# Kernel tuning notes

Hardware: AMD Instinct MI355X
Metric: run time of the kernel (lower is better)

## Reference

```python
import jax, jax.numpy as jnp
import numpy as np
from jax import lax

# Model hyperparameters (from module source: D_state=2, Expand=1; mamba-ssm defaults)
B_, C_, H_, W_ = 16, 128, 96, 96
D_MODEL = C_
D_INNER = 1 * D_MODEL          # expand = 1
D_STATE = 2
DT_RANK = (D_MODEL + 15) // 16  # ceil(d_model/16) = 8
D_CONV = 4
OUT_C = 128
LN_EPS = 1e-5


def setup_inputs() -> dict:
    key = jax.random.key(0)
    ks = jax.random.split(key, 10)
    s = 0.02
    x = jax.random.normal(ks[0], (B_, C_, H_, W_), dtype=jnp.float32)
    in_proj_w = jax.random.normal(ks[1], (2 * D_INNER, D_MODEL), dtype=jnp.float32) * s
    conv_w = jax.random.normal(ks[2], (D_INNER, 1, D_CONV), dtype=jnp.float32) * s
    conv_b = jnp.zeros((D_INNER,), dtype=jnp.float32)
    x_proj_w = jax.random.normal(ks[3], (DT_RANK + 2 * D_STATE, D_INNER), dtype=jnp.float32) * s
    dt_proj_w = jax.random.normal(ks[4], (D_INNER, DT_RANK), dtype=jnp.float32) * s
    # softplus^{-1}(0.01) so initial dt ~ 0.01 (standard mamba init)
    dt_proj_b = jnp.full((D_INNER,), float(np.log(np.expm1(0.01))), dtype=jnp.float32)
    A_log = jnp.log(jnp.broadcast_to(jnp.arange(1, D_STATE + 1, dtype=jnp.float32), (D_INNER, D_STATE)))
    D_param = jnp.ones((D_INNER,), dtype=jnp.float32)
    out_proj_w = jax.random.normal(ks[5], (OUT_C, D_INNER), dtype=jnp.float32) * s
    ln_gamma = jnp.ones((OUT_C,), dtype=jnp.float32)
    ln_beta = jnp.zeros((OUT_C,), dtype=jnp.float32)
    return {
        "x": x, "in_proj_w": in_proj_w, "conv_w": conv_w, "conv_b": conv_b,
        "x_proj_w": x_proj_w, "dt_proj_w": dt_proj_w, "dt_proj_b": dt_proj_b,
        "A_log": A_log, "D_param": D_param, "out_proj_w": out_proj_w,
        "ln_gamma": ln_gamma, "ln_beta": ln_beta,
    }


def _ssm_cha(x, in_proj_w, conv_w, conv_b, x_proj_w, dt_proj_w, dt_proj_b,
             A_log, D_param, out_proj_w, ln_gamma, ln_beta):
    b, c, h, w = x.shape
    L = h * w
    tokens = x.transpose(0, 2, 3, 1).reshape(b, L, c)  # [b, L, d_model]

    # in_proj -> (x_in, z)
    xz = jnp.einsum("bld,ed->ble", tokens, in_proj_w)  # [b, L, 2*d_inner]
    x_in, z = jnp.split(xz, 2, axis=-1)

    # causal depthwise conv1d over L, then SiLU
    xc = x_in.transpose(0, 2, 1)  # [b, d_inner, L]
    xc = lax.conv_general_dilated(
        xc, conv_w, window_strides=(1,), padding=[(D_CONV - 1, 0)],
        dimension_numbers=("NCH", "OIH", "NCH"), feature_group_count=D_INNER,
    ) + conv_b[None, :, None]
    x_in = jax.nn.silu(xc).transpose(0, 2, 1)  # [b, L, d_inner]

    # x_proj -> (dt, B, C)
    x_dbl = jnp.einsum("bld,ed->ble", x_in, x_proj_w)
    dt = x_dbl[..., :DT_RANK]
    Bc = x_dbl[..., DT_RANK:DT_RANK + D_STATE]         # [b, L, n]
    Cc = x_dbl[..., DT_RANK + D_STATE:]                # [b, L, n]
    dt = jax.nn.softplus(jnp.einsum("blr,dr->bld", dt, dt_proj_w) + dt_proj_b)

    # selective scan (diagonal A) via associative scan over L
    A = -jnp.exp(A_log)                                # [d_inner, n]
    dA = jnp.exp(dt[..., None] * A)                    # [b, L, d_inner, n]
    dBx = dt[..., None] * Bc[:, :, None, :] * x_in[..., None]

    def combine(e1, e2):
        a1, b1 = e1
        a2, b2 = e2
        return a1 * a2, a2 * b1 + b2

    _, hstate = lax.associative_scan(combine, (dA, dBx), axis=1)  # [b, L, d, n]
    y = jnp.sum(hstate * Cc[:, :, None, :], axis=-1) + D_param * x_in  # [b, L, d]

    y = y * jax.nn.silu(z)
    out = jnp.einsum("bld,od->blo", y, out_proj_w)     # [b, L, out_c]

    # LayerNorm over out_c
    mu = jnp.mean(out, axis=-1, keepdims=True)
    var = jnp.mean(jnp.square(out - mu), axis=-1, keepdims=True)
    out = (out - mu) * lax.rsqrt(var + LN_EPS) * ln_gamma + ln_beta

    return out.reshape(b, h, w, OUT_C).transpose(0, 3, 1, 2)


def reference(x, in_proj_w, conv_w, conv_b, x_proj_w, dt_proj_w, dt_proj_b,
              A_log, D_param, out_proj_w, ln_gamma, ln_beta):
    return _ssm_cha(x, in_proj_w, conv_w, conv_b, x_proj_w, dt_proj_w, dt_proj_b,
                    A_log, D_param, out_proj_w, ln_gamma, ln_beta)
```

## Files before the change

kernel.cpp:

```cpp
#include <hip/hip_runtime.h>
#include <hip/hip_bf16.h>
#include <hip/hip_fp16.h>

#define B_N 16
#define L_N 9216
#define LT64 144

typedef __attribute__((ext_vector_type(8))) short short8;
typedef __attribute__((ext_vector_type(4))) float floatx4;

__device__ __forceinline__ float bfu(unsigned short u) {
  return __uint_as_float(((unsigned int)u) << 16);
}
__device__ __forceinline__ unsigned short fbf(float f) {
  __hip_bfloat16 h = __float2bfloat16(f);
  return *(unsigned short*)&h;
}
__device__ __forceinline__ unsigned short fh(float f) {
  __half h = __float2half(f);
  return *(unsigned short*)&h;
}
__device__ __forceinline__ float hfu(unsigned short u) {
  __half h = *(__half*)&u;
  return __half2float(h);
}

__global__ __launch_bounds__(256) void k_prep(const float* __restrict__ w1,
                                              const float* __restrict__ w2,
                                              __hip_bfloat16* __restrict__ w1bt,
                                              __hip_bfloat16* __restrict__ w2bt) {
  int i = blockIdx.x * 256 + threadIdx.x;
  if (i < 256 * 128) w1bt[i] = __float2bfloat16(w1[i]);
  if (i < 128 * 128) w2bt[i] = __float2bfloat16(w2[i]);
}

__global__ __launch_bounds__(512, 4) void k_inproj_conv(
    const float* __restrict__ x, const __hip_bfloat16* __restrict__ w1bt,
    const float* __restrict__ cw, const float* __restrict__ cb,
    const float* __restrict__ xpw, const float* __restrict__ dtw,
    const float* __restrict__ dtb,
    __hip_bfloat16* __restrict__ xinb, __hip_bfloat16* __restrict__ zb,
    float* __restrict__ xdbl4, unsigned short* __restrict__ dth) {
  __shared__ __align__(16) char smem1[16384];
  __shared__ __align__(16) char smem2[34816];
  unsigned short* xs = (unsigned short*)smem1;
  unsigned short* xe = (unsigned short*)smem2;
  float (*cvs)[68] = (float(*)[68])smem2;
  float (*red)[12][64] = (float(*)[12][64])smem2;

  int blk = blockIdx.x, b = blk / LT64, lt = blk % LT64, l0 = lt * 64;
  int t = threadIdx.x;
  int lane = t & 63, wv = t >> 6;
  int col = lane & 15, quad = lane >> 4;

  const float* xb = x + (size_t)b * 128 * L_N + l0 - 16;
#pragma unroll
  for (int i = 0; i < 5; ++i) {
    int idx = t + i * 512;
    int c = idx & 127, q = idx >> 7;
    float4 v = {0.f, 0.f, 0.f, 0.f};
    if (!(lt == 0 && q < 4)) v = *(const float4*)(xb + (size_t)c * L_N + q * 4);
    int ch = c >> 3, ce = c & 7;
    if (q < 4) {
#pragma unroll
      for (int j = 0; j < 4; ++j) {
        int l = q * 4 + j;
        xe[l * 128 + (((ch ^ (l & 7)) << 3) | ce)] = fbf(((const float*)&v)[j]);
      }
    } else {
#pragma unroll
      for (int j = 0; j < 4; ++j) {
        int l = q * 4 - 16 + j;
        xs[l * 128 + (((ch ^ (l & 7)) << 3) | ce)] = fbf(((const float*)&v)[j]);
      }
    }
  }

  int e0 = wv * 32;
  const __hip_bfloat16* wbp = w1bt + (size_t)(e0 + col) * 128 + quad * 8;
  floatx4 vzero = {0.f, 0.f, 0.f, 0.f};
  floatx4 acc[2][5];
#pragma unroll
  for (int mi = 0; mi < 2; ++mi)
#pragma unroll
    for (int ni = 0; ni < 5; ++ni) acc[mi][ni] = vzero;
  short8 a0 = *(const short8*)(wbp);
  short8 a1 = *(const short8*)(wbp + 16 * 128);
  __syncthreads();

#pragma unroll
  for (int ks = 0; ks < 4; ++ks) {
    short8 n0, n1;
    if (ks < 3) {
      n0 = *(const short8*)(wbp + (ks + 1) * 32);
      n1 = *(const short8*)(wbp + 16 * 128 + (ks + 1) * 32);
    }
    short8 bfr[5];
    bfr[0] = *(const short8*)&xe[col * 128 + (((ks * 4 + quad) ^ (col & 7)) << 3)];
#pragma unroll
    for (int ni = 1; ni < 5; ++ni) {
      int row = (ni - 1) * 16 + col;
      bfr[ni] = *(const short8*)&xs[row * 128 + (((ks * 4 + quad) ^ (row & 7)) << 3)];
    }
#pragma unroll
    for (int ni = 0; ni < 5; ++ni) {
      acc[0][ni] = __builtin_amdgcn_mfma_f32_16x16x32_bf16(a0, bfr[ni], acc[0][ni], 0, 0, 0);
      acc[1][ni] = __builtin_amdgcn_mfma_f32_16x16x32_bf16(a1, bfr[ni], acc[1][ni], 0, 0, 0);
    }
    a0 = n0; a1 = n1;
  }
  __syncthreads();

  if (wv >= 4) {
    __hip_bfloat16* zbase = zb + ((size_t)b * 128 + (e0 - 128)) * L_N + l0;
#pragma unroll
    for (int mi = 0; mi < 2; ++mi)
#pragma unroll
      for (int r = 0; r < 4; ++r) {
        int dr = mi * 16 + quad * 4 + r;
#pragma unroll
        for (int ni = 1; ni < 5; ++ni)
          zbase[(size_t)dr * L_N + (ni - 1) * 16 + col] = __float2bfloat16(acc[mi][ni][r]);
      }
  } else {
#pragma unroll
    for (int mi = 0; mi < 2; ++mi)
#pragma unroll
      for (int r = 0; r < 4; ++r) {
        int d = e0 + mi * 16 + quad * 4 + r;
        if (col >= 13) cvs[d][col - 13] = acc[mi][0][r];
#pragma unroll
        for (int ni = 1; ni < 5; ++ni) cvs[d][3 + (ni - 1) * 16 + col] = acc[mi][ni][r];
      }
  }
  __syncthreads();

  float part[12];
#pragma unroll
  for (int m = 0; m < 12; ++m) part[m] = 0.f;
  for (int dd = 0; dd < 16; ++dd) {
    int d = wv * 16 + dd;
    float v = cb[d] + cw[d * 4 + 0] * cvs[d][lane] + cw[d * 4 + 1] * cvs[d][lane + 1]
                    + cw[d * 4 + 2] * cvs[d][lane + 2] + cw[d * 4 + 3] * cvs[d][lane + 3];
    v = v / (1.f + __expf(-v));
    xinb[((size_t)b * 128 + d) * L_N + l0 + lane] = __float2bfloat16(v);
#pragma unroll
    for (int m = 0; m < 12; ++m) part[m] += xpw[m * 128 + d] * v;
  }
  __syncthreads();
#pragma unroll
  for (int m = 0; m < 12; ++m) red[wv][m][lane] = part[m];
  __syncthreads();
  for (int idx = t; idx < 12 * 64; idx += 512) {
    int m = idx >> 6, l = idx & 63;
    float s = 0.f;
#pragma unroll
    for (int w8 = 0; w8 < 8; ++w8) s += red[w8][m][l];
    red[0][m][l] = s;
    if (m >= 8) xdbl4[((size_t)b * 4 + (m - 8)) * L_N + l0 + l] = s;
  }
  __syncthreads();
  for (int dd = 0; dd < 16; ++dd) {
    int d = wv * 16 + dd;
    float p = dtb[d];
#pragma unroll
    for (int r = 0; r < 8; ++r) p += dtw[d * 8 + r] * red[0][r][lane];
    float dt = (p > 15.f) ? p : __logf(1.f + __expf(p));
    dth[((size_t)b * 128 + d) * L_N + l0 + lane] = fh(dt);
  }
}

__global__ __launch_bounds__(256) void k_scan(
    const float* __restrict__ xdbl4, const unsigned short* __restrict__ dth,
    const float* __restrict__ alog, const float* __restrict__ dpar,
    const __hip_bfloat16* __restrict__ xinb, const __hip_bfloat16* __restrict__ zb,
    __hip_bfloat16* __restrict__ yb) {
  __shared__ float agg[4][4];
  __shared__ float carry[2];
  int blk = blockIdx.x, b = blk >> 7, d = blk & 127;
  int t = threadIdx.x, lane = t & 63, wv = t >> 6;
  float A0 = -__expf(alog[2 * d]), A1 = -__expf(alog[2 * d + 1]);
  float Dv = dpar[d];
  if (t == 0) { carry[0] = 0.f; carry[1] = 0.f; }
  __syncthreads();
  const float* xdT = xdbl4 + (size_t)b * 4 * L_N;
  const unsigned short* dtp_ = dth + ((size_t)b * 128 + d) * L_N;
  const unsigned short* xi = (const unsigned short*)xinb + ((size_t)b * 128 + d) * L_N;
  const unsigned short* zr = (const unsigned short*)zb + ((size_t)b * 128 + d) * L_N;
  unsigned short* yo = (unsigned short*)yb + ((size_t)b * 128 + d) * L_N;
  for (int it = 0; it < 9; ++it) {
    int lb = it * 1024 + t * 4;
    float4 q[4];
#pragma unroll
    for (int m = 0; m < 4; ++m) q[m] = *(const float4*)(xdT + (size_t)m * L_N + lb);
    ushort4 du = *(const ushort4*)(dtp_ + lb);
    ushort4 xu = *(const ushort4*)(xi + lb);
    ushort4 zu = *(const ushort4*)(zr + lb);
    float dtv[4] = {hfu(du.x), hfu(du.y), hfu(du.z), hfu(du.w)};
    float xv[4] = {bfu(xu.x), bfu(xu.y), bfu(xu.z), bfu(xu.w)};
    float zv[4] = {bfu(zu.x), bfu(zu.y), bfu(zu.z), bfu(zu.w)};
    float A0p[4], X0p[4], A1p[4], X1p[4];
#pragma unroll
    for (int j = 0; j < 4; ++j) {
      float dt = dtv[j];
      float a0 = __expf(dt * A0), a1 = __expf(dt * A1);
      float dtx = dt * xv[j];
      float x0 = dtx * ((const float*)&q[0])[j];
      float x1 = dtx * ((const float*)&q[1])[j];
      if (j == 0) { A0p[0] = a0; X0p[0] = x0; A1p[0] = a1; X1p[0] = x1; }
      else {
        A0p[j] = a0 * A0p[j - 1]; X0p[j] = a0 * X0p[j - 1] + x0;
        A1p[j] = a1 * A1p[j - 1]; X1p[j] = a1 * X1p[j - 1] + x1;
      }
    }
    float wA0 = A0p[3], wX0 = X0p[3], wA1 = A1p[3], wX1 = X1p[3];
#pragma unroll
    for (int off = 1; off < 64; off <<= 1) {
      float pA0 = __shfl_up(wA0, off, 64), pX0 = __shfl_up(wX0, off, 64);
      float pA1 = __shfl_up(wA1, off, 64), pX1 = __shfl_up(wX1, off, 64);
      if (lane >= off) {
        wX0 += wA0 * pX0; wA0 *= pA0;
        wX1 += wA1 * pX1; wA1 *= pA1;
      }
    }
    if (lane == 63) { agg[wv][0] = wA0; agg[wv][1] = wX0; agg[wv][2] = wA1; agg[wv][3] = wX1; }
    float eA0 = __shfl_up(wA0, 1, 64), eX0 = __shfl_up(wX0, 1, 64);
    float eA1 = __shfl_up(wA1, 1, 64), eX1 = __shfl_up(wX1, 1, 64);
    if (lane == 0) { eA0 = 1.f; eX0 = 0.f; eA1 = 1.f; eX1 = 0.f; }
    __syncthreads();
    float h0 = carry[0], h1 = carry[1];
    for (int jw = 0; jw < wv; ++jw) {
      h0 = agg[jw][0] * h0 + agg[jw][1];
      h1 = agg[jw][2] * h1 + agg[jw][3];
    }
    h0 = eA0 * h0 + eX0;
    h1 = eA1 * h1 + eX1;
    __syncthreads();
    if (t == 255) { carry[0] = A0p[3] * h0 + X0p[3]; carry[1] = A1p[3] * h1 + X1p[3]; }
    ushort4 yu;
    unsigned short* yp = (unsigned short*)&yu;
#pragma unroll
    for (int j = 0; j < 4; ++j) {
      float hh0 = A0p[j] * h0 + X0p[j];
      float hh1 = A1p[j] * h1 + X1p[j];
      float y = hh0 * ((const float*)&q[2])[j] + hh1 * ((const float*)&q[3])[j] + Dv * xv[j];
      y *= zv[j] / (1.f + __expf(-zv[j]));
      yp[j] = fbf(y);
    }
    *(ushort4*)(yo + lb) = yu;
  }
}

__global__ __launch_bounds__(256) void k_outln(
    const __hip_bfloat16* __restrict__ yb, const __hip_bfloat16* __restrict__ w2bt,
    const float* __restrict__ gam, const float* __restrict__ bet,
    float* __restrict__ out) {
  __shared__ unsigned short st[128][68];
  __shared__ __hip_bfloat16 yts[64 * 128];
  __shared__ float red_s[4][64], red_q[4][64];
  __shared__ float gs[128], bs[128];
  int blk = blockIdx.x, b = blk / LT64, lt = blk % LT64, l0 = lt * 64;
  int t = threadIdx.x;
  if (t < 128) { gs[t] = gam[t]; bs[t] = bet[t]; }
  const unsigned short* ybb = (const unsigned short*)yb + (size_t)b * 128 * L_N + l0;
#pragma unroll
  for (int i = 0; i < 8; ++i) {
    int idx = t + i * 256;
    int dd = idx >> 4, l4 = (idx & 15) * 4;
    ushort4 v = *(const ushort4*)(ybb + (size_t)dd * L_N + l4);
    *(ushort4*)&st[dd][l4] = v;
  }
  __syncthreads();
#pragma unroll
  for (int p = 0; p < 4; ++p) {
    int gi = t + p * 256;
    int l = gi & 63, ch = gi >> 6;
    short8 c;
#pragma unroll
    for (int j = 0; j < 8; ++j) c[j] = (short)st[ch * 8 + j][l];
    *(short8*)&yts[l * 128 + ((ch ^ (l & 7)) * 8)] = c;
  }
  int lane = t & 63, wv = t >> 6;
  int col = lane & 15, quad = lane >> 4;
  int o0 = wv * 32;
  short8 afr[2][4];
#pragma unroll
  for (int mi = 0; mi < 2; ++mi)
#pragma unroll
    for (int ks = 0; ks < 4; ++ks)
      afr[mi][ks] = *(const short8*)(w2bt + (size_t)(o0 + mi * 16 + col) * 128 + ks * 32 + quad * 8);
  floatx4 vzero = {0.f, 0.f, 0.f, 0.f};
  floatx4 acc[2][4];
#pragma unroll
  for (int mi = 0; mi < 2; ++mi)
#pragma unroll
    for (int ni = 0; ni < 4; ++ni) acc[mi][ni] = vzero;
  __syncthreads();
#pragma unroll
  for (int ks = 0; ks < 4; ++ks) {
    short8 bfr[4];
#pragma unroll
    for (int ni = 0; ni < 4; ++ni) {
      int row = ni * 16 + col;
      bfr[ni] = *(const short8*)&yts[row * 128 + (((ks * 4 + quad) ^ (row & 7)) * 8)];
    }
#pragma unroll
    for (int mi = 0; mi < 2; ++mi)
#pragma unroll
      for (int ni = 0; ni < 4; ++ni)
        acc[mi][ni] = __builtin_amdgcn_mfma_f32_16x16x32_bf16(afr[mi][ks], bfr[ni], acc[mi][ni], 0, 0, 0);
  }
  float s[4], q[4];
#pragma unroll
  for (int ni = 0; ni < 4; ++ni) {
    float ss = 0.f, qq = 0.f;
#pragma unroll
    for (int mi = 0; mi < 2; ++mi)
#pragma unroll
      for (int r = 0; r < 4; ++r) {
        float v = acc[mi][ni][r];
        ss += v; qq += v * v;
      }
    ss += __shfl_xor(ss, 16, 64); ss += __shfl_xor(ss, 32, 64);
    qq += __shfl_xor(qq, 16, 64); qq += __shfl_xor(qq, 32, 64);
    s[ni] = ss; q[ni] = qq;
  }
  if (quad == 0) {
#pragma unroll
    for (int ni = 0; ni < 4; ++ni) {
      red_s[wv][ni * 16 + col] = s[ni];
      red_q[wv][ni * 16 + col] = q[ni];
    }
  }
  __syncthreads();
  float mu[4], rstd[4];
#pragma unroll
  for (int ni = 0; ni < 4; ++ni) {
    int li = ni * 16 + col;
    float ts = red_s[0][li] + red_s[1][li] + red_s[2][li] + red_s[3][li];
    float tq = red_q[0][li] + red_q[1][li] + red_q[2][li] + red_q[3][li];
    float m = ts * (1.f / 128.f);
    float var = tq * (1.f / 128.f) - m * m;
    mu[ni] = m;
    rstd[ni] = rsqrtf(var + 1e-5f);
  }
  float* ob = out + (size_t)b * 128 * L_N;
#pragma unroll
  for (int mi = 0; mi < 2; ++mi)
#pragma unroll
    for (int r = 0; r < 4; ++r) {
      int o = o0 + mi * 16 + quad * 4 + r;
      float g = gs[o], bb = bs[o];
#pragma unroll
      for (int ni = 0; ni < 4; ++ni)
        ob[(size_t)o * L_N + l0 + ni * 16 + col] = (acc[mi][ni][r] - mu[ni]) * rstd[ni] * g + bb;
    }
}

extern "C" void kernel_launch(void* const* d_in, const int* in_sizes, int n_in,
                              void* d_out, int out_size, void* d_ws, size_t ws_size,
                              hipStream_t stream) {
  const float* x    = (const float*)d_in[0];
  const float* w1   = (const float*)d_in[1];
  const float* cw   = (const float*)d_in[2];
  const float* cb   = (const float*)d_in[3];
  const float* xpw  = (const float*)d_in[4];
  const float* dtw  = (const float*)d_in[5];
  const float* dtb  = (const float*)d_in[6];
  const float* alog = (const float*)d_in[7];
  const float* dpar = (const float*)d_in[8];
  const float* w2   = (const float*)d_in[9];
  const float* gam  = (const float*)d_in[10];
  const float* bet  = (const float*)d_in[11];
  float* out = (float*)d_out;

  float* ws = (float*)d_ws;
  const size_t NBL = (size_t)B_N * 128 * L_N;
  float* xdbl4 = ws;
  unsigned short* dth = (unsigned short*)(ws + (size_t)B_N * 4 * L_N);
  __hip_bfloat16* xinb = (__hip_bfloat16*)(dth + NBL);
  __hip_bfloat16* zb   = xinb + NBL;
  __hip_bfloat16* yb   = zb + NBL;
  __hip_bfloat16* w1bt = yb + NBL;
  __hip_bfloat16* w2bt = w1bt + 256 * 128;

  k_prep<<<128, 256, 0, stream>>>(w1, w2, w1bt, w2bt);
  k_inproj_conv<<<B_N * LT64, 512, 0, stream>>>(x, w1bt, cw, cb, xpw, dtw, dtb,
                                                xinb, zb, xdbl4, dth);
  k_scan<<<B_N * 128, 256, 0, stream>>>(xdbl4, dth, alog, dpar, xinb, zb, yb);
  k_outln<<<B_N * LT64, 256, 0, stream>>>(yb, w2bt, gam, bet, out);
}
```

Measured before the change: 300.7 us.

## Shrink conv staging to fp16, use atomic LDS reduction, double-buffer scan carry

In the in-proj/conv kernel, the conv staging buffer is stored as fp16 instead of fp32, which shrinks shared memory and should allow more resident blocks. The per-wave partial sums for x_proj are combined with LDS atomicAdd into one zeroed 12x64 buffer, replacing a staged 8-way reduction and two barriers. In the scan kernel, the aggregate and carry arrays are double-buffered by iteration parity, which removes one __syncthreads per iteration. The fp16 staging adds rounding error to the conv input, and the LDS atomics may serialize.

```diff
diff --git a/kernel.cpp b/kernel.cpp
--- a/kernel.cpp
+++ b/kernel.cpp
@@ -42,16 +42,22 @@
     __hip_bfloat16* __restrict__ xinb, __hip_bfloat16* __restrict__ zb,
     float* __restrict__ xdbl4, unsigned short* __restrict__ dth) {
   __shared__ __align__(16) char smem1[16384];
-  __shared__ __align__(16) char smem2[34816];
+  __shared__ __align__(16) char smem2[18432];
+  __shared__ __align__(16) float red[12][64];
   unsigned short* xs = (unsigned short*)smem1;
   unsigned short* xe = (unsigned short*)smem2;
-  float (*cvs)[68] = (float(*)[68])smem2;
-  float (*red)[12][64] = (float(*)[12][64])smem2;
+  unsigned short (*cvs)[72] = (unsigned short(*)[72])smem2;
 
   int blk = blockIdx.x, b = blk / LT64, lt = blk % LT64, l0 = lt * 64;
   int t = threadIdx.x;
   int lane = t & 63, wv = t >> 6;
   int col = lane & 15, quad = lane >> 4;
+
+  {
+    float* rf = (float*)red;
+    rf[t] = 0.f;
+    if (t < 256) rf[512 + t] = 0.f;
+  }
 
   const float* xb = x + (size_t)b * 128 * L_N + l0 - 16;
 #pragma unroll
@@ -128,9 +134,9 @@
 #pragma unroll
       for (int r = 0; r < 4; ++r) {
         int d = e0 + mi * 16 + quad * 4 + r;
-        if (col >= 13) cvs[d][col - 13] = acc[mi][0][r];
-#pragma unroll
-        for (int ni = 1; ni < 5; ++ni) cvs[d][3 + (ni - 1) * 16 + col] = acc[mi][ni][r];
+        if (col >= 13) cvs[d][col - 13] = fh(acc[mi][0][r]);
+#pragma unroll
+        for (int ni = 1; ni < 5; ++ni) cvs[d][3 + (ni - 1) * 16 + col] = fh(acc[mi][ni][r]);
       }
   }
   __syncthreads();
@@ -140,31 +146,29 @@
   for (int m = 0; m < 12; ++m) part[m] = 0.f;
   for (int dd = 0; dd < 16; ++dd) {
     int d = wv * 16 + dd;
-    float v = cb[d] + cw[d * 4 + 0] * cvs[d][lane] + cw[d * 4 + 1] * cvs[d][lane + 1]
-                    + cw[d * 4 + 2] * cvs[d][lane + 2] + cw[d * 4 + 3] * cvs[d][lane + 3];
+    float v = cb[d] + cw[d * 4 + 0] * hfu(cvs[d][lane]) + cw[d * 4 + 1] * hfu(cvs[d][lane + 1])
+                    + cw[d * 4 + 2] * hfu(cvs[d][lane + 2]) + cw[d * 4 + 3] * hfu(cvs[d][lane + 3]);
     v = v / (1.f + __expf(-v));
     xinb[((size_t)b * 128 + d) * L_N + l0 + lane] = __float2bfloat16(v);
 #pragma unroll
     for (int m = 0; m < 12; ++m) part[m] += xpw[m * 128 + d] * v;
   }
-  __syncthreads();
-#pragma unroll
-  for (int m = 0; m < 12; ++m) red[wv][m][lane] = part[m];
-  __syncthreads();
-  for (int idx = t; idx < 12 * 64; idx += 512) {
-    int m = idx >> 6, l = idx & 63;
-    float s = 0.f;
-#pragma unroll
-    for (int w8 = 0; w8 < 8; ++w8) s += red[w8][m][l];
-    red[0][m][l] = s;
-    if (m >= 8) xdbl4[((size_t)b * 4 + (m - 8)) * L_N + l0 + l] = s;
-  }
-  __syncthreads();
+#pragma unroll
+  for (int m = 0; m < 12; ++m) atomicAdd(&red[m][lane], part[m]);
+  __syncthreads();
+
+  if (t < 256) {
+    int m = 8 + (t >> 6), l = t & 63;
+    xdbl4[((size_t)b * 4 + (m - 8)) * L_N + l0 + l] = red[m][l];
+  }
+  float xd[8];
+#pragma unroll
+  for (int r = 0; r < 8; ++r) xd[r] = red[r][lane];
   for (int dd = 0; dd < 16; ++dd) {
     int d = wv * 16 + dd;
     float p = dtb[d];
 #pragma unroll
-    for (int r = 0; r < 8; ++r) p += dtw[d * 8 + r] * red[0][r][lane];
+    for (int r = 0; r < 8; ++r) p += dtw[d * 8 + r] * xd[r];
     float dt = (p > 15.f) ? p : __logf(1.f + __expf(p));
     dth[((size_t)b * 128 + d) * L_N + l0 + lane] = fh(dt);
   }
@@ -175,13 +179,13 @@
     const float* __restrict__ alog, const float* __restrict__ dpar,
     const __hip_bfloat16* __restrict__ xinb, const __hip_bfloat16* __restrict__ zb,
     __hip_bfloat16* __restrict__ yb) {
-  __shared__ float agg[4][4];
-  __shared__ float carry[2];
+  __shared__ float agg[2][4][4];
+  __shared__ float carry[2][2];
   int blk = blockIdx.x, b = blk >> 7, d = blk & 127;
   int t = threadIdx.x, lane = t & 63, wv = t >> 6;
   float A0 = -__expf(alog[2 * d]), A1 = -__expf(alog[2 * d + 1]);
   float Dv = dpar[d];
-  if (t == 0) { carry[0] = 0.f; carry[1] = 0.f; }
+  if (t == 0) { carry[0][0] = 0.f; carry[0][1] = 0.f; }
   __syncthreads();
   const float* xdT = xdbl4 + (size_t)b * 4 * L_N;
   const unsigned short* dtp_ = dth + ((size_t)b * 128 + d) * L_N;
@@ -189,6 +193,7 @@
   const unsigned short* zr = (const unsigned short*)zb + ((size_t)b * 128 + d) * L_N;
   unsigned short* yo = (unsigned short*)yb + ((size_t)b * 128 + d) * L_N;
   for (int it = 0; it < 9; ++it) {
+    int p = it & 1;
     int lb = it * 1024 + t * 4;
     float4 q[4];
 #pragma unroll
@@ -223,20 +228,22 @@
         wX1 += wA1 * pX1; wA1 *= pA1;
       }
     }
-    if (lane == 63) { agg[wv][0] = wA0; agg[wv][1] = wX0; agg[wv][2] = wA1; agg[wv][3] = wX1; }
+    if (lane == 63) { agg[p][wv][0] = wA0; agg[p][wv][1] = wX0; agg[p][wv][2] = wA1; agg[p][wv][3] = wX1; }
     float eA0 = __shfl_up(wA0, 1, 64), eX0 = __shfl_up(wX0, 1, 64);
     float eA1 = __shfl_up(wA1, 1, 64), eX1 = __shfl_up(wX1, 1, 64);
     if (lane == 0) { eA0 = 1.f; eX0 = 0.f; eA1 = 1.f; eX1 = 0.f; }
     __syncthreads();
-    float h0 = carry[0], h1 = carry[1];
+    float h0 = carry[p][0], h1 = carry[p][1];
     for (int jw = 0; jw < wv; ++jw) {
-      h0 = agg[jw][0] * h0 + agg[jw][1];
-      h1 = agg[jw][2] * h1 + agg[jw][3];
+      h0 = agg[p][jw][0] * h0 + agg[p][jw][1];
+      h1 = agg[p][jw][2] * h1 + agg[p][jw][3];
     }
     h0 = eA0 * h0 + eX0;
     h1 = eA1 * h1 + eX1;
-    __syncthreads();
-    if (t == 255) { carry[0] = A0p[3] * h0 + X0p[3]; carry[1] = A1p[3] * h1 + X1p[3]; }
+    if (t == 255) {
+      carry[p ^ 1][0] = A0p[3] * h0 + X0p[3];
+      carry[p ^ 1][1] = A1p[3] * h1 + X1p[3];
+    }
     ushort4 yu;
     unsigned short* yp = (unsigned short*)&yu;
 #pragma unroll
```

After: 362.0 us. 20.4% more time.
